# Kernel optimization log

Measured on AMD Instinct MI355X. Metric: run time of the kernel, lower is better.

The kernel has to match this reference:

```python
import jax, jax.numpy as jnp
import numpy as np

EPS = 1e-05
NEG = -1e9

def rotate_half(x):
    x1, x2 = jnp.split(x, 2, axis=-1)
    return jnp.concatenate([-x2, x1], axis=-1)

def rmsnorm(x, w):
    xf = x.astype(jnp.float32)
    n = xf * jax.lax.rsqrt(jnp.mean(xf * xf, axis=-1, keepdims=True) + EPS)
    return w * n.astype(x.dtype)

def setup_inputs() -> dict:
    key = jax.random.key(0)
    ks = jax.random.split(key, 12)
    B, S, H, NH, DH, FF = 1, 2048, 2048, 16, 128, 8192
    x = jax.random.normal(ks[0], (B, S, H), jnp.float32)
    # additive causal mask [1,1,S,S]
    causal = jnp.where(jnp.tril(jnp.ones((S, S), bool)), 0.0, NEG).astype(jnp.float32)
    attention_mask = causal[None, None]
    alibi = 0.1 * jax.random.normal(ks[1], (1, NH, S, S), jnp.float32)
    # rotary angles [S, DH]
    inv = 1.0 / (10000.0 ** (jnp.arange(0, DH, 2, dtype=jnp.float32) / DH))
    ang = jnp.arange(S, dtype=jnp.float32)[:, None] * inv[None, :]
    freqs = jnp.concatenate([ang, ang], axis=-1)  # [S, DH]
    sc = 1.0 / np.sqrt(H)
    wq = sc * jax.random.normal(ks[2], (H, H), jnp.float32)
    wk = sc * jax.random.normal(ks[3], (H, H), jnp.float32)
    wv = sc * jax.random.normal(ks[4], (H, H), jnp.float32)
    wo = sc * jax.random.normal(ks[5], (H, H), jnp.float32)
    w1 = sc * jax.random.normal(ks[6], (H, FF), jnp.float32)
    w3 = sc * jax.random.normal(ks[7], (H, FF), jnp.float32)
    w2 = (1.0 / np.sqrt(FF)) * jax.random.normal(ks[8], (FF, H), jnp.float32)
    attn_norm_w = jnp.ones((H,), jnp.float32)
    ffn_norm_w = jnp.ones((H,), jnp.float32)
    return dict(x=x, attention_mask=attention_mask, alibi=alibi, freqs=freqs,
                wq=wq, wk=wk, wv=wv, wo=wo, w1=w1, w2=w2, w3=w3,
                attn_norm_w=attn_norm_w, ffn_norm_w=ffn_norm_w)

def reference(x, attention_mask, alibi, freqs, wq, wk, wv, wo, w1, w2, w3,
              attn_norm_w, ffn_norm_w):
    B, S, H = x.shape
    NH = 16
    DH = H // NH
    nx = rmsnorm(x, attn_norm_w)
    # projections -> [B, NH, S, DH]
    def heads(y):
        return y.reshape(B, S, NH, DH).transpose(0, 2, 1, 3)
    q = heads(nx @ wq)
    k = heads(nx @ wk)
    v = heads(nx @ wv)
    cos, sin = jnp.cos(freqs), jnp.sin(freqs)  # [S, DH] broadcasts over B,NH
    q = q * cos + rotate_half(q) * sin
    k = k * cos + rotate_half(k) * sin
    scores = jnp.einsum('bhqd,bhkd->bhqk', q, k) / np.sqrt(DH)
    scores = scores + attention_mask + alibi
    attn = jax.nn.softmax(scores, axis=-1)
    out = jnp.einsum('bhqk,bhkd->bhqd', attn, v)
    out = out.transpose(0, 2, 1, 3).reshape(B, S, H)
    x = x + out @ wo
    nx = rmsnorm(x, ffn_norm_w)
    ff = (jax.nn.silu(nx @ w1) * (nx @ w3)) @ w2
    return x + ff
```

## Files before the change

### kernel.cpp

```cpp
#include <hip/hip_runtime.h>
#include <hip/hip_bf16.h>
#include <math.h>

typedef __bf16 bf16x8 __attribute__((ext_vector_type(8)));
typedef float  f32x4  __attribute__((ext_vector_type(4)));
typedef unsigned short u16x8 __attribute__((ext_vector_type(8)));

#define DEV static __device__ __forceinline__

DEV void gload16(const void* g, void* l) {
  __builtin_amdgcn_global_load_lds((__attribute__((address_space(1))) void*)g,
                                   (__attribute__((address_space(3))) void*)l,
                                   16, 0, 0);
}

DEV float bf2f(unsigned short u) {
  unsigned v = ((unsigned)u) << 16;
  return __builtin_bit_cast(float, v);
}
DEV unsigned short f2bf(float f) {
  unsigned u = __builtin_bit_cast(unsigned, f);
  u = u + 0x7fffu + ((u >> 16) & 1u);
  return (unsigned short)(u >> 16);
}

__global__ __launch_bounds__(256) void rmsnorm_k(const float* __restrict__ x,
    const float* __restrict__ w, unsigned short* __restrict__ out, int H) {
  int row = blockIdx.x;
  const float4* xr = (const float4*)(x + (size_t)row * H);
  float4 a = xr[threadIdx.x * 2], b = xr[threadIdx.x * 2 + 1];
  float ss = a.x*a.x + a.y*a.y + a.z*a.z + a.w*a.w
           + b.x*b.x + b.y*b.y + b.z*b.z + b.w*b.w;
#pragma unroll
  for (int o = 32; o; o >>= 1) ss += __shfl_down(ss, o, 64);
  __shared__ float red[4];
  if ((threadIdx.x & 63) == 0) red[threadIdx.x >> 6] = ss;
  __syncthreads();
  float rs = rsqrtf((red[0] + red[1] + red[2] + red[3]) * (1.0f / 2048.0f) + 1e-5f);
  size_t base = (size_t)row * H + threadIdx.x * 8;
  const float* wv = w + threadIdx.x * 8;
  float vals[8] = {a.x, a.y, a.z, a.w, b.x, b.y, b.z, b.w};
  u16x8 o8;
#pragma unroll
  for (int i = 0; i < 8; ++i) o8[i] = f2bf(vals[i] * rs * wv[i]);
  *(u16x8*)(out + base) = o8;
}

__global__ __launch_bounds__(256) void wtrans_k(const float* __restrict__ W,
    unsigned short* __restrict__ Wt, int R, int C) {
  __shared__ float tile[32][33];
  int c0 = blockIdx.x * 32, r0 = blockIdx.y * 32;
  int tx = threadIdx.x, ty = threadIdx.y;
#pragma unroll
  for (int i = 0; i < 4; ++i)
    tile[ty + i * 8][tx] = W[(size_t)(r0 + ty + i * 8) * C + c0 + tx];
  __syncthreads();
#pragma unroll
  for (int i = 0; i < 4; ++i)
    Wt[(size_t)(c0 + ty + i * 8) * R + r0 + tx] = f2bf(tile[tx][ty + i * 8]);
}


#define STG_A(H, BUF, KC) do {                                                 \
    gload16(Asrc0 + (size_t)(H) * 128 * lda + (KC),                            \
            &lds[(BUF) * 16384 + (H) * 8192 + w * 1024]);                      \
    gload16(Asrc1 + (size_t)(H) * 128 * lda + (KC),                            \
            &lds[(BUF) * 16384 + (H) * 8192 + w * 1024 + 512]);                \
  } while (0)

#define STG_B(H, BUF, KC) do {                                                 \
    gload16(Bsrc0 + (size_t)(H) * 128 * ldb + (KC),                            \
            &lds[32768 + (BUF) * 16384 + (H) * 8192 + w * 1024]);              \
    gload16(Bsrc1 + (size_t)(H) * 128 * ldb + (KC),                            \
            &lds[32768 + (BUF) * 16384 + (H) * 8192 + w * 1024 + 512]);        \
  } while (0)

#define DS_A(DST, MH) do {                                                     \
    const int abase = buf * 16384 + (MH) * 8192 + arow * 64;                   \
    _Pragma("unroll") for (int m = 0; m < 4; ++m) {                            \
      DST[m][0] = *(const bf16x8*)&lds[abase + m * 1024 + acol0];              \
      DST[m][1] = *(const bf16x8*)&lds[abase + m * 1024 + acol1];              \
    } } while (0)

#define DS_B(DST, NH) do {                                                     \
    const int bbase = 32768 + buf * 16384 + (NH) * 8192 + brow * 64;           \
    _Pragma("unroll") for (int n = 0; n < 2; ++n) {                            \
      DST[n][0] = *(const bf16x8*)&lds[bbase + n * 1024 + acol0];              \
      DST[n][1] = *(const bf16x8*)&lds[bbase + n * 1024 + acol1];              \
    } } while (0)

#define MFMA16(AI, AR, BR) do {                                                \
    __builtin_amdgcn_s_setprio(1);                                             \
    _Pragma("unroll") for (int m = 0; m < 4; ++m)                              \
      _Pragma("unroll") for (int n = 0; n < 2; ++n) {                          \
        acc[AI][m][n] = __builtin_amdgcn_mfma_f32_16x16x32_bf16(               \
            AR[m][0], BR[n][0], acc[AI][m][n], 0, 0, 0);                       \
        acc[AI][m][n] = __builtin_amdgcn_mfma_f32_16x16x32_bf16(               \
            AR[m][1], BR[n][1], acc[AI][m][n], 0, 0, 0);                       \
      }                                                                        \
    __builtin_amdgcn_s_setprio(0);                                             \
    __builtin_amdgcn_sched_barrier(0);                                         \
  } while (0)

#define SBAR_WAIT do {                                                         \
    __builtin_amdgcn_sched_barrier(0);                                         \
    __builtin_amdgcn_s_barrier();                                              \
    asm volatile("s_waitcnt lgkmcnt(0)" ::: "memory");                         \
  } while (0)

template <int EPI>
__global__ __launch_bounds__(512, 2) void gemm256_k(
    const unsigned short* __restrict__ A, int lda,
    const unsigned short* __restrict__ B, int ldb,
    unsigned short* __restrict__ Cb, float* __restrict__ Cf,
    int M, int N, int Kext) {
  __shared__ unsigned short lds[65536];
  const int t = threadIdx.x, w = t >> 6, lane = t & 63;
  const int nbm = M >> 8, nbn = N >> 8, nwg = nbm * nbn;
  int id = blockIdx.x;
  id = (id & 7) * (nwg >> 3) + (id >> 3);
  const int bm = id % nbm, bn = id / nbm;
  const size_t m0 = (size_t)bm << 8, n0 = (size_t)bn << 8;
  const int koff = blockIdx.y * Kext;
  const int NT = Kext >> 6;
  const int scol = ((lane & 7) ^ (lane >> 3)) * 8;
  const unsigned short* Asrc0 = A + (m0 + w * 16 + (lane >> 3)) * (size_t)lda + koff + scol;
  const unsigned short* Asrc1 = A + (m0 + w * 16 + 8 + (lane >> 3)) * (size_t)lda + koff + scol;
  const unsigned short* Bsrc0 = B + (n0 + w * 16 + (lane >> 3)) * (size_t)ldb + koff + scol;
  const unsigned short* Bsrc1 = B + (n0 + w * 16 + 8 + (lane >> 3)) * (size_t)ldb + koff + scol;
  const int arow = (w >> 2) * 64 + (lane & 15);
  const int brow = (w & 3) * 32 + (lane & 15);
  const int acol0 = ((lane >> 4) * 8) ^ ((lane & 7) << 3);
  const int acol1 = acol0 ^ 32;
  f32x4 acc[4][4][2] = {};
  bf16x8 Acur[4][2], B0r[2][2], B1r[2][2];
  STG_A(0, 0, 0); STG_B(0, 0, 0); STG_A(1, 0, 0); STG_B(1, 0, 0);
  STG_A(0, 1, 64); STG_B(0, 1, 64);
  asm volatile("s_waitcnt vmcnt(4)" ::: "memory");
  __builtin_amdgcn_s_barrier();
  for (int kt = 0; kt < NT; ++kt) {
    const int buf = kt & 1;
    const int kc1 = (kt + 1) * 64, kc2 = (kt + 2) * 64;
    const bool p1 = (kt + 1 < NT), p2 = (kt + 2 < NT);
    DS_A(Acur, 0); DS_B(B0r, 0);
    if (p1) STG_A(1, buf ^ 1, kc1);
    SBAR_WAIT;
    MFMA16(0, Acur, B0r);
    __builtin_amdgcn_s_barrier();
    DS_B(B1r, 1);
    if (p1) STG_B(1, buf ^ 1, kc1);
    SBAR_WAIT;
    MFMA16(1, Acur, B1r);
    __builtin_amdgcn_s_barrier();
    DS_A(Acur, 1);
    if (p2) STG_A(0, buf, kc2);
    SBAR_WAIT;
    MFMA16(3, Acur, B1r);
    __builtin_amdgcn_s_barrier();
    if (p2) STG_B(0, buf, kc2);
    __builtin_amdgcn_sched_barrier(0);
    __builtin_amdgcn_s_barrier();
    MFMA16(2, Acur, B0r);
    if (p2) { asm volatile("s_waitcnt vmcnt(4)" ::: "memory"); }
    else    { asm volatile("s_waitcnt vmcnt(0)" ::: "memory"); }
    __builtin_amdgcn_s_barrier();
  }
#pragma unroll
  for (int Mh = 0; Mh < 2; ++Mh)
#pragma unroll
    for (int Nh = 0; Nh < 2; ++Nh)
#pragma unroll
      for (int m = 0; m < 4; ++m)
#pragma unroll
        for (int n = 0; n < 2; ++n) {
          size_t gr = m0 + Mh * 128 + (w >> 2) * 64 + m * 16 + (lane >> 4) * 4;
          size_t gc = n0 + Nh * 128 + (w & 3) * 32 + n * 16 + (lane & 15);
          f32x4 v = acc[Mh * 2 + Nh][m][n];
#pragma unroll
          for (int j = 0; j < 4; ++j) {
            size_t o = (gr + j) * (size_t)N + gc;
            if constexpr (EPI == 0) Cb[o] = f2bf(v[j]);
            else Cf[(size_t)blockIdx.y * M * N + o] = v[j];
          }
        }
}

template <int EPI>
__global__ __launch_bounds__(256) void gemm_bt_k(
    const unsigned short* __restrict__ A, const unsigned short* __restrict__ B,
    float* __restrict__ Cf, unsigned short* __restrict__ Cb,
    const float* __restrict__ resid, int M, int N, int K) {
  constexpr int BK = 64;
  __shared__ unsigned short lA[128 * BK];
  __shared__ unsigned short lB[128 * BK];
  const int t = threadIdx.x, wave = t >> 6, lane = t & 63;
  int nwg = gridDim.x * gridDim.y;
  int id = blockIdx.y * gridDim.x + blockIdx.x;
  id = (id & 7) * (nwg >> 3) + (id >> 3);
  const int m0 = (id % gridDim.x) * 128, n0 = (id / gridDim.x) * 128;
  const int wr = (wave >> 1) * 64, wc = (wave & 1) * 64;
  f32x4 acc[4][4] = {};
  const int sr = t >> 3;
  const int sc = ((t & 7) ^ (sr & 7)) * 8;
  const unsigned short* Ab = A + (size_t)(m0 + sr) * K + sc;
  const unsigned short* Bb = B + (size_t)(n0 + sr) * K + sc;
  unsigned short* lAw = &lA[(wave * 8) * BK];
  unsigned short* lBw = &lB[(wave * 8) * BK];
  const int row = lane & 15, kg = (lane >> 4) * 8, swz = (lane & 7) << 3;
  for (int k0 = 0; k0 < K; k0 += BK) {
#pragma unroll
    for (int it = 0; it < 4; ++it) {
      gload16(Ab + (size_t)it * 32 * K + k0, lAw + it * 32 * BK);
      gload16(Bb + (size_t)it * 32 * K + k0, lBw + it * 32 * BK);
    }
    asm volatile("s_waitcnt vmcnt(0)" ::: "memory");
    __syncthreads();
#pragma unroll
    for (int kk = 0; kk < 2; ++kk) {
      bf16x8 af[4], bfr[4];
#pragma unroll
      for (int m = 0; m < 4; ++m)
        af[m] = *(const bf16x8*)&lA[(wr + m * 16 + row) * BK + ((kk * 32 + kg) ^ swz)];
#pragma unroll
      for (int n = 0; n < 4; ++n)
        bfr[n] = *(const bf16x8*)&lB[(wc + n * 16 + row) * BK + ((kk * 32 + kg) ^ swz)];
#pragma unroll
      for (int m = 0; m < 4; ++m)
#pragma unroll
        for (int n = 0; n < 4; ++n)
          acc[m][n] = __builtin_amdgcn_mfma_f32_16x16x32_bf16(af[m], bfr[n], acc[m][n], 0, 0, 0);
    }
    __syncthreads();
  }
  const int cg = lane >> 4, col = lane & 15;
#pragma unroll
  for (int m = 0; m < 4; ++m)
#pragma unroll
    for (int n = 0; n < 4; ++n) {
      int rr = m0 + wr + m * 16 + cg * 4;
      int cc = n0 + wc + n * 16 + col;
#pragma unroll
      for (int j = 0; j < 4; ++j) {
        float v = acc[m][n][j];
        size_t o = (size_t)(rr + j) * N + cc;
        if constexpr (EPI == 2) Cf[o] = v + resid[o];
        else if constexpr (EPI == 1) Cf[o] = v;
        else Cb[o] = f2bf(v);
      }
    }
}

__global__ __launch_bounds__(256) void rope_k(const unsigned short* __restrict__ qkv,
    const float* __restrict__ freqs, unsigned short* __restrict__ Qr,
    unsigned short* __restrict__ Kr, int S) {
  int idx = blockIdx.x * 256 + threadIdx.x;
  int dp = idx & 63, h = (idx >> 6) & 15, s = idx >> 10;
  float ang = freqs[s * 128 + dp];
  float c, sn;
  sincosf(ang, &sn, &c);
  size_t rq = (size_t)s * 6144 + h * 128 + dp;
  float q1 = bf2f(qkv[rq]),        q2 = bf2f(qkv[rq + 64]);
  float k1 = bf2f(qkv[rq + 2048]), k2 = bf2f(qkv[rq + 2048 + 64]);
  size_t ob = ((size_t)h * S + s) * 128 + dp;
  Qr[ob]      = f2bf(q1 * c - q2 * sn);
  Qr[ob + 64] = f2bf(q2 * c + q1 * sn);
  Kr[ob]      = f2bf(k1 * c - k2 * sn);
  Kr[ob + 64] = f2bf(k2 * c + k1 * sn);
}

__global__ __launch_bounds__(256) void vtrans_k(const unsigned short* __restrict__ qkv,
    unsigned short* __restrict__ Vt, int S) {
  __shared__ unsigned short tile[32][33];
  int h = blockIdx.z;
  int s0 = blockIdx.x * 32, d0 = blockIdx.y * 32;
  int tx = threadIdx.x, ty = threadIdx.y;
#pragma unroll
  for (int i = 0; i < 4; ++i)
    tile[ty + i * 8][tx] = qkv[(size_t)(s0 + ty + i * 8) * 6144 + 4096 + h * 128 + d0 + tx];
  __syncthreads();
#pragma unroll
  for (int i = 0; i < 4; ++i)
    Vt[((size_t)h * 128 + d0 + ty + i * 8) * S + s0 + tx] = tile[tx][ty + i * 8];
}

__global__ __launch_bounds__(256) void attn_k(
    const unsigned short* __restrict__ Qr, const unsigned short* __restrict__ Kr,
    const unsigned short* __restrict__ Vt, const float* __restrict__ alibi,
    unsigned short* __restrict__ Ao, int S) {
  const int DH = 128;
  __shared__ unsigned short lQ[64 * 128], lK[64 * 128], lV[128 * 64], lP[4 * 16 * 64];
  const int t = threadIdx.x, wave = t >> 6, lane = t & 63;
  const int h = blockIdx.y;
  const int nq = gridDim.x;
  const int bx = blockIdx.x;
  const int qt = (bx & 1) ? (nq - 1 - (bx >> 1)) : (bx >> 1);
  const int q0 = qt * 64;
  const int sr = t >> 4;
  const int scw = ((t & 15) ^ ((t >> 4) & 7)) * 8;
  const int vr = t >> 3;
  const int vcw = ((t & 7) ^ ((t >> 3) & 7)) * 8;
  const unsigned short* Qb = Qr + (size_t)h * S * DH;
  const unsigned short* Kb = Kr + (size_t)h * S * DH;
  const unsigned short* Vb = Vt + (size_t)h * DH * S;
#pragma unroll
  for (int it = 0; it < 4; ++it)
    gload16(Qb + (size_t)(q0 + it * 16 + sr) * DH + scw, &lQ[(it * 16 + wave * 4) * DH]);
  asm volatile("s_waitcnt vmcnt(0)" ::: "memory");
  __syncthreads();
  const int row = lane & 15, kg = (lane >> 4) * 8, cg = lane >> 4, col = lane & 15;
  const int kswz = (lane & 7) << 3;
  bf16x8 qf[4];
#pragma unroll
  for (int ks = 0; ks < 4; ++ks)
    qf[ks] = *(const bf16x8*)&lQ[(wave * 16 + row) * DH + ((ks * 32 + kg) ^ kswz)];
  f32x4 o[8] = {};
  float m_run[4] = {-1e30f, -1e30f, -1e30f, -1e30f};
  float l_run[4] = {};
  unsigned short* pw = &lP[wave * 16 * 64];
  const float scale = 0.08838834764831843f;
  const int ktiles = qt + 1;
  for (int kt = 0; kt < ktiles; ++kt) {
    int k0 = kt * 64;
#pragma unroll
    for (int it = 0; it < 4; ++it)
      gload16(Kb + (size_t)(k0 + it * 16 + sr) * DH + scw, &lK[(it * 16 + wave * 4) * DH]);
#pragma unroll
    for (int it = 0; it < 4; ++it)
      gload16(Vb + (size_t)(it * 32 + vr) * S + k0 + vcw, &lV[(it * 32 + wave * 8) * 64]);
    asm volatile("s_waitcnt vmcnt(4)" ::: "memory");
    __syncthreads();
    float al[4][4];
#pragma unroll
    for (int n = 0; n < 4; ++n) {
      int k_abs = k0 + n * 16 + col;
#pragma unroll
      for (int j = 0; j < 4; ++j) {
        int q_abs = q0 + wave * 16 + cg * 4 + j;
        al[n][j] = alibi[((size_t)h * S + q_abs) * S + k_abs];
      }
    }
    f32x4 sf[4] = {};
#pragma unroll
    for (int ks = 0; ks < 4; ++ks) {
      bf16x8 qv = qf[ks];
#pragma unroll
      for (int n = 0; n < 4; ++n) {
        bf16x8 kf = *(const bf16x8*)&lK[(n * 16 + row) * DH + ((ks * 32 + kg) ^ kswz)];
        sf[n] = __builtin_amdgcn_mfma_f32_16x16x32_bf16(qv, kf, sf[n], 0, 0, 0);
      }
    }
    float pv[4][4];
    float tmax[4] = {-1e30f, -1e30f, -1e30f, -1e30f};
#pragma unroll
    for (int n = 0; n < 4; ++n) {
      int k_abs = k0 + n * 16 + col;
#pragma unroll
      for (int j = 0; j < 4; ++j) {
        int q_abs = q0 + wave * 16 + cg * 4 + j;
        float v = sf[n][j] * scale + al[n][j];
        if (k_abs > q_abs) v = -1e30f;
        pv[n][j] = v;
        tmax[j] = fmaxf(tmax[j], v);
      }
    }
#pragma unroll
    for (int o2 = 1; o2 < 16; o2 <<= 1)
#pragma unroll
      for (int j = 0; j < 4; ++j) tmax[j] = fmaxf(tmax[j], __shfl_xor(tmax[j], o2, 64));
    float alpha[4], rsum[4] = {};
#pragma unroll
    for (int j = 0; j < 4; ++j) {
      float mn = fmaxf(m_run[j], tmax[j]);
      alpha[j] = __expf(m_run[j] - mn);
      m_run[j] = mn;
    }
#pragma unroll
    for (int n = 0; n < 4; ++n)
#pragma unroll
      for (int j = 0; j < 4; ++j) {
        float p = __expf(pv[n][j] - m_run[j]);
        pv[n][j] = p;
        rsum[j] += p;
      }
#pragma unroll
    for (int o2 = 1; o2 < 16; o2 <<= 1)
#pragma unroll
      for (int j = 0; j < 4; ++j) rsum[j] += __shfl_xor(rsum[j], o2, 64);
#pragma unroll
    for (int j = 0; j < 4; ++j) l_run[j] = l_run[j] * alpha[j] + rsum[j];
#pragma unroll
    for (int nn = 0; nn < 8; ++nn)
#pragma unroll
      for (int j = 0; j < 4; ++j) o[nn][j] *= alpha[j];
#pragma unroll
    for (int n = 0; n < 4; ++n)
#pragma unroll
      for (int j = 0; j < 4; ++j) {
        int pr = cg * 4 + j;
        pw[pr * 64 + ((n * 16 + col) ^ ((pr & 7) << 3))] = f2bf(pv[n][j]);
      }
    asm volatile("s_waitcnt vmcnt(0)" ::: "memory");
    __syncthreads();
#pragma unroll
    for (int kk = 0; kk < 2; ++kk) {
      bf16x8 pf = *(const bf16x8*)&pw[row * 64 + ((kk * 32 + kg) ^ kswz)];
#pragma unroll
      for (int nn = 0; nn < 8; ++nn) {
        bf16x8 vf = *(const bf16x8*)&lV[(nn * 16 + row) * 64 + ((kk * 32 + kg) ^ kswz)];
        o[nn] = __builtin_amdgcn_mfma_f32_16x16x32_bf16(pf, vf, o[nn], 0, 0, 0);
      }
    }
    __syncthreads();
  }
#pragma unroll
  for (int nn = 0; nn < 8; ++nn)
#pragma unroll
    for (int j = 0; j < 4; ++j) {
      int q_abs = q0 + wave * 16 + cg * 4 + j;
      Ao[(size_t)q_abs * 2048 + h * 128 + nn * 16 + col] = f2bf(o[nn][j] / l_run[j]);
    }
}

__global__ __launch_bounds__(256) void silumul2_k(const unsigned short* __restrict__ h13,
    unsigned short* __restrict__ g, long n8) {
  long i = (long)blockIdx.x * 256 + threadIdx.x;
  if (i >= n8) return;
  int rowi = (int)(i >> 10), c = (int)(i & 1023) * 8;
  u16x8 a = *(const u16x8*)(h13 + (size_t)rowi * 16384 + c);
  u16x8 b = *(const u16x8*)(h13 + (size_t)rowi * 16384 + 8192 + c);
  u16x8 r;
#pragma unroll
  for (int j = 0; j < 8; ++j) {
    float xx = bf2f(a[j]), yy = bf2f(b[j]);
    float s = xx / (1.0f + __expf(-xx));
    r[j] = f2bf(s * yy);
  }
  *(u16x8*)(g + i * 8) = r;
}

__global__ __launch_bounds__(256) void reduce4_k(const float* __restrict__ part,
    const float* __restrict__ resid, float* __restrict__ out, int n4, size_t mn) {
  int i = blockIdx.x * 256 + threadIdx.x;
  if (i >= n4) return;
  const float4* p = (const float4*)part;
  size_t q = mn >> 2;
  float4 a = ((const float4*)resid)[i];
  float4 s0 = p[i], s1 = p[i + q], s2 = p[i + 2 * q], s3 = p[i + 3 * q];
  float4 r;
  r.x = a.x + s0.x + s1.x + s2.x + s3.x;
  r.y = a.y + s0.y + s1.y + s2.y + s3.y;
  r.z = a.z + s0.z + s1.z + s2.z + s3.z;
  r.w = a.w + s0.w + s1.w + s2.w + s3.w;
  ((float4*)out)[i] = r;
}

extern "C" void kernel_launch(void* const* d_in, const int* in_sizes, int n_in,
                              void* d_out, int out_size, void* d_ws, size_t ws_size,
                              hipStream_t stream) {
  const int S = 2048, H = 2048, NH = 16, DH = 128, FF = 8192;
  const float* x     = (const float*)d_in[0];
  const float* alibi = (const float*)d_in[2];
  const float* freqs = (const float*)d_in[3];
  const float* wq    = (const float*)d_in[4];
  const float* wk    = (const float*)d_in[5];
  const float* wv    = (const float*)d_in[6];
  const float* wo    = (const float*)d_in[7];
  const float* w1    = (const float*)d_in[8];
  const float* w2    = (const float*)d_in[9];
  const float* w3    = (const float*)d_in[10];
  const float* anw   = (const float*)d_in[11];
  const float* fnw   = (const float*)d_in[12];
  float* out = (float*)d_out;

  char* ws = (char*)d_ws;
  size_t off = 0;
  auto alloc = [&](size_t n) { char* p = ws + off; off += (n + 255) & ~(size_t)255; return p; };
  unsigned short* qkvT = (unsigned short*)alloc((size_t)3 * H * H * 2);
  unsigned short* woT  = (unsigned short*)alloc((size_t)H * H * 2);
  unsigned short* w13T = (unsigned short*)alloc((size_t)2 * FF * H * 2);
  unsigned short* w2T  = (unsigned short*)alloc((size_t)H * FF * 2);
  float*          x2   = (float*)alloc((size_t)S * H * 4);
  unsigned short* nx2  = (unsigned short*)alloc((size_t)S * H * 2);
  unsigned short* gbuf = (unsigned short*)alloc((size_t)S * FF * 2);
  unsigned short* nx   = (unsigned short*)alloc((size_t)S * H * 2);
  unsigned short* qkvb = (unsigned short*)alloc((size_t)S * 3 * H * 2);
  unsigned short* Qr   = (unsigned short*)alloc((size_t)NH * S * DH * 2);
  unsigned short* Kr   = (unsigned short*)alloc((size_t)NH * S * DH * 2);
  unsigned short* Vt   = (unsigned short*)alloc((size_t)NH * DH * S * 2);
  unsigned short* attno= (unsigned short*)alloc((size_t)S * H * 2);
  unsigned short* h13  = nx;
  float* part = (float*)ws;

  dim3 tb32(32, 8);
  wtrans_k<<<dim3(64, 64), tb32, 0, stream>>>(wq, qkvT, H, H);
  wtrans_k<<<dim3(64, 64), tb32, 0, stream>>>(wk, qkvT + (size_t)H * H, H, H);
  wtrans_k<<<dim3(64, 64), tb32, 0, stream>>>(wv, qkvT + (size_t)2 * H * H, H, H);
  wtrans_k<<<dim3(64, 64), tb32, 0, stream>>>(wo, woT, H, H);
  wtrans_k<<<dim3(256, 64), tb32, 0, stream>>>(w1, w13T, H, FF);
  wtrans_k<<<dim3(256, 64), tb32, 0, stream>>>(w3, w13T + (size_t)FF * H, H, FF);
  wtrans_k<<<dim3(64, 256), tb32, 0, stream>>>(w2, w2T, FF, H);

  rmsnorm_k<<<S, 256, 0, stream>>>(x, anw, nx, H);
  gemm256_k<0><<<dim3(192, 1), 512, 0, stream>>>(nx, H, qkvT, H, qkvb, nullptr, S, 3 * H, H);
  rope_k<<<(S * NH * 64) / 256, 256, 0, stream>>>(qkvb, freqs, Qr, Kr, S);
  vtrans_k<<<dim3(S / 32, DH / 32, NH), tb32, 0, stream>>>(qkvb, Vt, S);
  attn_k<<<dim3(S / 64, NH), 256, 0, stream>>>(Qr, Kr, Vt, alibi, attno, S);
  gemm_bt_k<2><<<dim3(16, 16), 256, 0, stream>>>(attno, woT, x2, nullptr, x, S, H, H);
  rmsnorm_k<<<S, 256, 0, stream>>>(x2, fnw, nx2, H);
  gemm256_k<0><<<dim3(512, 1), 512, 0, stream>>>(nx2, H, w13T, H, h13, nullptr, S, 2 * FF, H);
  silumul2_k<<<8192, 256, 0, stream>>>(h13, gbuf, (long)S * FF / 8);
  gemm256_k<1><<<dim3(64, 4), 512, 0, stream>>>(gbuf, FF, w2T, FF, nullptr, part, S, H, H);
  reduce4_k<<<4096, 256, 0, stream>>>(part, x2, out, S * H / 4, (size_t)S * H);
}
```

Before: 568.7 us.

## Fuse SiLU-gate into W1/W3 GEMM epilogue and double-buffer attention K/V loads

Interleaves the transposed W1 and W3 rows in 16-row groups so each GEMM output tile holds matching gate and up columns. A new GEMM epilogue then applies SiLU and the multiply directly and writes the gated result, which removes the separate silumul kernel and the round trip of the 2×FF intermediate through memory. The attention kernel is also restructured to double-buffer K/V tiles in LDS and prefetch the next tile's alibi values into registers. Q is loaded straight from global memory into registers. This adds register pressure and more complex vmcnt accounting.

```diff
diff --git a/kernel.cpp b/kernel.cpp
--- a/kernel.cpp
+++ b/kernel.cpp
@@ -58,6 +58,23 @@
 #pragma unroll
   for (int i = 0; i < 4; ++i)
     Wt[(size_t)(c0 + ty + i * 8) * R + r0 + tx] = f2bf(tile[tx][ty + i * 8]);
+}
+
+__global__ __launch_bounds__(256) void wtrans_ilv_k(const float* __restrict__ W,
+    unsigned short* __restrict__ Wt, int R, int C, int half) {
+  __shared__ float tile[32][33];
+  int c0 = blockIdx.x * 32, r0 = blockIdx.y * 32;
+  int tx = threadIdx.x, ty = threadIdx.y;
+#pragma unroll
+  for (int i = 0; i < 4; ++i)
+    tile[ty + i * 8][tx] = W[(size_t)(r0 + ty + i * 8) * C + c0 + tx];
+  __syncthreads();
+#pragma unroll
+  for (int i = 0; i < 4; ++i) {
+    int c = c0 + ty + i * 8;
+    size_t dstrow = (size_t)(c >> 4) * 32 + (c & 15) + half * 16;
+    Wt[dstrow * R + r0 + tx] = f2bf(tile[tx][ty + i * 8]);
+  }
 }
 
 
@@ -170,19 +187,31 @@
 #pragma unroll
     for (int Nh = 0; Nh < 2; ++Nh)
 #pragma unroll
-      for (int m = 0; m < 4; ++m)
-#pragma unroll
-        for (int n = 0; n < 2; ++n) {
-          size_t gr = m0 + Mh * 128 + (w >> 2) * 64 + m * 16 + (lane >> 4) * 4;
-          size_t gc = n0 + Nh * 128 + (w & 3) * 32 + n * 16 + (lane & 15);
-          f32x4 v = acc[Mh * 2 + Nh][m][n];
+      for (int m = 0; m < 4; ++m) {
+        size_t gr = m0 + Mh * 128 + (w >> 2) * 64 + m * 16 + (lane >> 4) * 4;
+        if constexpr (EPI == 2) {
+          size_t gc = (n0 >> 1) + Nh * 64 + (w & 3) * 16 + (lane & 15);
+          f32x4 v0 = acc[Mh * 2 + Nh][m][0];
+          f32x4 v1 = acc[Mh * 2 + Nh][m][1];
 #pragma unroll
           for (int j = 0; j < 4; ++j) {
-            size_t o = (gr + j) * (size_t)N + gc;
-            if constexpr (EPI == 0) Cb[o] = f2bf(v[j]);
-            else Cf[(size_t)blockIdx.y * M * N + o] = v[j];
+            float s = v0[j] / (1.0f + __expf(-v0[j]));
+            Cb[(gr + j) * (size_t)(N >> 1) + gc] = f2bf(s * v1[j]);
+          }
+        } else {
+#pragma unroll
+          for (int n = 0; n < 2; ++n) {
+            size_t gc = n0 + Nh * 128 + (w & 3) * 32 + n * 16 + (lane & 15);
+            f32x4 v = acc[Mh * 2 + Nh][m][n];
+#pragma unroll
+            for (int j = 0; j < 4; ++j) {
+              size_t o = (gr + j) * (size_t)N + gc;
+              if constexpr (EPI == 0) Cb[o] = f2bf(v[j]);
+              else Cf[(size_t)blockIdx.y * M * N + o] = v[j];
+            }
           }
         }
+      }
 }
 
 template <int EPI>
@@ -283,134 +312,121 @@
     Vt[((size_t)h * 128 + d0 + ty + i * 8) * S + s0 + tx] = tile[tx][ty + i * 8];
 }
 
+
+#define STGKV(KT, BUF) do {                                                    \
+    _Pragma("unroll") for (int it = 0; it < 4; ++it)                           \
+      gload16(Kb + (size_t)((KT) * 64 + it * 16 + sr) * 128 + scw,             \
+              &lds[(BUF) * 8192 + (it * 16 + wave * 4) * 128]);                \
+    _Pragma("unroll") for (int it = 0; it < 4; ++it)                           \
+      gload16(Vb + (size_t)(it * 32 + vr) * S + (KT) * 64 + vcw,               \
+              &lds[16384 + (BUF) * 8192 + (it * 32 + wave * 8) * 64]);         \
+  } while (0)
+
+#define ATTN_TILE(CUR, NXT, KT) do {                                           \
+    const int buf = (KT) & 1;                                                  \
+    const bool p1 = ((KT) + 1 < ktiles);                                       \
+    if (p1) {                                                                  \
+      STGKV((KT) + 1, buf ^ 1);                                                \
+      _Pragma("unroll") for (int q8 = 0; q8 < 16; ++q8)                        \
+        NXT[q8] = albase[(size_t)(q8 & 3) * S + ((KT) + 1) * 64 + (q8 >> 2) * 16]; \
+      asm volatile("s_waitcnt vmcnt(24)" ::: "memory");                        \
+    } else {                                                                   \
+      asm volatile("s_waitcnt vmcnt(0)" ::: "memory");                         \
+    }                                                                          \
+    __builtin_amdgcn_s_barrier();                                              \
+    f32x4 sf[4] = {};                                                          \
+    _Pragma("unroll") for (int ks = 0; ks < 4; ++ks)                           \
+      _Pragma("unroll") for (int n = 0; n < 4; ++n) {                          \
+        bf16x8 kf = *(const bf16x8*)&lds[buf * 8192 + (n * 16 + row) * 128 +   \
+                                         ((ks * 32 + kg) ^ kswz)];             \
+        sf[n] = __builtin_amdgcn_mfma_f32_16x16x32_bf16(qf[ks], kf, sf[n], 0, 0, 0); \
+      }                                                                        \
+    float pv[4][4];                                                            \
+    float tmax[4] = {-1e30f, -1e30f, -1e30f, -1e30f};                          \
+    _Pragma("unroll") for (int n = 0; n < 4; ++n) {                            \
+      int k_abs = (KT) * 64 + n * 16 + col;                                    \
+      _Pragma("unroll") for (int j = 0; j < 4; ++j) {                          \
+        int q_abs = q0 + wave * 16 + cg * 4 + j;                               \
+        float v = sf[n][j] * scale + CUR[n * 4 + j];                           \
+        if (k_abs > q_abs) v = -1e30f;                                         \
+        pv[n][j] = v;                                                          \
+        tmax[j] = fmaxf(tmax[j], v);                                           \
+      } }                                                                      \
+    _Pragma("unroll") for (int o2 = 1; o2 < 16; o2 <<= 1)                      \
+      _Pragma("unroll") for (int j = 0; j < 4; ++j)                            \
+        tmax[j] = fmaxf(tmax[j], __shfl_xor(tmax[j], o2, 64));                 \
+    float alpha[4], rsum[4] = {};                                              \
+    _Pragma("unroll") for (int j = 0; j < 4; ++j) {                            \
+      float mn = fmaxf(m_run[j], tmax[j]);                                     \
+      alpha[j] = __expf(m_run[j] - mn);                                        \
+      m_run[j] = mn;                                                           \
+    }                                                                          \
+    _Pragma("unroll") for (int n = 0; n < 4; ++n)                              \
+      _Pragma("unroll") for (int j = 0; j < 4; ++j) {                          \
+        float p = __expf(pv[n][j] - m_run[j]);                                 \
+        pv[n][j] = p;                                                          \
+        rsum[j] += p;                                                          \
+      }                                                                        \
+    _Pragma("unroll") for (int o2 = 1; o2 < 16; o2 <<= 1)                      \
+      _Pragma("unroll") for (int j = 0; j < 4; ++j)                            \
+        rsum[j] += __shfl_xor(rsum[j], o2, 64);                                \
+    _Pragma("unroll") for (int j = 0; j < 4; ++j)                              \
+      l_run[j] = l_run[j] * alpha[j] + rsum[j];                                \
+    _Pragma("unroll") for (int nn = 0; nn < 8; ++nn)                           \
+      _Pragma("unroll") for (int j = 0; j < 4; ++j) o[nn][j] *= alpha[j];      \
+    _Pragma("unroll") for (int n = 0; n < 4; ++n)                              \
+      _Pragma("unroll") for (int j = 0; j < 4; ++j) {                          \
+        int pr = cg * 4 + j;                                                   \
+        pw[pr * 64 + ((n * 16 + col) ^ ((pr & 7) << 3))] = f2bf(pv[n][j]);     \
+      }                                                                        \
+    asm volatile("s_waitcnt lgkmcnt(0)" ::: "memory");                         \
+    __builtin_amdgcn_sched_barrier(0);                                         \
+    _Pragma("unroll") for (int kk = 0; kk < 2; ++kk) {                         \
+      bf16x8 pf = *(const bf16x8*)&pw[row * 64 + ((kk * 32 + kg) ^ kswz)];     \
+      _Pragma("unroll") for (int nn = 0; nn < 8; ++nn) {                       \
+        bf16x8 vf = *(const bf16x8*)&lds[16384 + buf * 8192 +                  \
+                                         (nn * 16 + row) * 64 +                \
+                                         ((kk * 32 + kg) ^ kswz)];             \
+        o[nn] = __builtin_amdgcn_mfma_f32_16x16x32_bf16(pf, vf, o[nn], 0, 0, 0); \
+      } }                                                                      \
+    __builtin_amdgcn_s_barrier();                                              \
+  } while (0)
+
 __global__ __launch_bounds__(256) void attn_k(
     const unsigned short* __restrict__ Qr, const unsigned short* __restrict__ Kr,
     const unsigned short* __restrict__ Vt, const float* __restrict__ alibi,
     unsigned short* __restrict__ Ao, int S) {
-  const int DH = 128;
-  __shared__ unsigned short lQ[64 * 128], lK[64 * 128], lV[128 * 64], lP[4 * 16 * 64];
+  __shared__ unsigned short lds[36864];
   const int t = threadIdx.x, wave = t >> 6, lane = t & 63;
-  const int h = blockIdx.y;
-  const int nq = gridDim.x;
-  const int bx = blockIdx.x;
+  const int h = blockIdx.y, nq = gridDim.x, bx = blockIdx.x;
   const int qt = (bx & 1) ? (nq - 1 - (bx >> 1)) : (bx >> 1);
   const int q0 = qt * 64;
-  const int sr = t >> 4;
-  const int scw = ((t & 15) ^ ((t >> 4) & 7)) * 8;
-  const int vr = t >> 3;
-  const int vcw = ((t & 7) ^ ((t >> 3) & 7)) * 8;
-  const unsigned short* Qb = Qr + (size_t)h * S * DH;
-  const unsigned short* Kb = Kr + (size_t)h * S * DH;
-  const unsigned short* Vb = Vt + (size_t)h * DH * S;
-#pragma unroll
-  for (int it = 0; it < 4; ++it)
-    gload16(Qb + (size_t)(q0 + it * 16 + sr) * DH + scw, &lQ[(it * 16 + wave * 4) * DH]);
-  asm volatile("s_waitcnt vmcnt(0)" ::: "memory");
-  __syncthreads();
+  const int sr = t >> 4, scw = ((t & 15) ^ ((t >> 4) & 7)) * 8;
+  const int vr = t >> 3, vcw = ((t & 7) ^ ((t >> 3) & 7)) * 8;
+  const unsigned short* Kb = Kr + (size_t)h * S * 128;
+  const unsigned short* Vb = Vt + (size_t)h * 128 * S;
   const int row = lane & 15, kg = (lane >> 4) * 8, cg = lane >> 4, col = lane & 15;
   const int kswz = (lane & 7) << 3;
   bf16x8 qf[4];
-#pragma unroll
-  for (int ks = 0; ks < 4; ++ks)
-    qf[ks] = *(const bf16x8*)&lQ[(wave * 16 + row) * DH + ((ks * 32 + kg) ^ kswz)];
+  const unsigned short* Qrow = Qr + ((size_t)h * S + q0 + wave * 16 + row) * 128;
+#pragma unroll
+  for (int ks = 0; ks < 4; ++ks) qf[ks] = *(const bf16x8*)&Qrow[ks * 32 + kg];
   f32x4 o[8] = {};
   float m_run[4] = {-1e30f, -1e30f, -1e30f, -1e30f};
   float l_run[4] = {};
-  unsigned short* pw = &lP[wave * 16 * 64];
+  unsigned short* pw = &lds[32768 + wave * 1024];
   const float scale = 0.08838834764831843f;
   const int ktiles = qt + 1;
-  for (int kt = 0; kt < ktiles; ++kt) {
-    int k0 = kt * 64;
-#pragma unroll
-    for (int it = 0; it < 4; ++it)
-      gload16(Kb + (size_t)(k0 + it * 16 + sr) * DH + scw, &lK[(it * 16 + wave * 4) * DH]);
-#pragma unroll
-    for (int it = 0; it < 4; ++it)
-      gload16(Vb + (size_t)(it * 32 + vr) * S + k0 + vcw, &lV[(it * 32 + wave * 8) * 64]);
-    asm volatile("s_waitcnt vmcnt(4)" ::: "memory");
-    __syncthreads();
-    float al[4][4];
-#pragma unroll
-    for (int n = 0; n < 4; ++n) {
-      int k_abs = k0 + n * 16 + col;
-#pragma unroll
-      for (int j = 0; j < 4; ++j) {
-        int q_abs = q0 + wave * 16 + cg * 4 + j;
-        al[n][j] = alibi[((size_t)h * S + q_abs) * S + k_abs];
-      }
-    }
-    f32x4 sf[4] = {};
-#pragma unroll
-    for (int ks = 0; ks < 4; ++ks) {
-      bf16x8 qv = qf[ks];
-#pragma unroll
-      for (int n = 0; n < 4; ++n) {
-        bf16x8 kf = *(const bf16x8*)&lK[(n * 16 + row) * DH + ((ks * 32 + kg) ^ kswz)];
-        sf[n] = __builtin_amdgcn_mfma_f32_16x16x32_bf16(qv, kf, sf[n], 0, 0, 0);
-      }
-    }
-    float pv[4][4];
-    float tmax[4] = {-1e30f, -1e30f, -1e30f, -1e30f};
-#pragma unroll
-    for (int n = 0; n < 4; ++n) {
-      int k_abs = k0 + n * 16 + col;
-#pragma unroll
-      for (int j = 0; j < 4; ++j) {
-        int q_abs = q0 + wave * 16 + cg * 4 + j;
-        float v = sf[n][j] * scale + al[n][j];
-        if (k_abs > q_abs) v = -1e30f;
-        pv[n][j] = v;
-        tmax[j] = fmaxf(tmax[j], v);
-      }
-    }
-#pragma unroll
-    for (int o2 = 1; o2 < 16; o2 <<= 1)
-#pragma unroll
-      for (int j = 0; j < 4; ++j) tmax[j] = fmaxf(tmax[j], __shfl_xor(tmax[j], o2, 64));
-    float alpha[4], rsum[4] = {};
-#pragma unroll
-    for (int j = 0; j < 4; ++j) {
-      float mn = fmaxf(m_run[j], tmax[j]);
-      alpha[j] = __expf(m_run[j] - mn);
-      m_run[j] = mn;
-    }
-#pragma unroll
-    for (int n = 0; n < 4; ++n)
-#pragma unroll
-      for (int j = 0; j < 4; ++j) {
-        float p = __expf(pv[n][j] - m_run[j]);
-        pv[n][j] = p;
-        rsum[j] += p;
-      }
-#pragma unroll
-    for (int o2 = 1; o2 < 16; o2 <<= 1)
-#pragma unroll
-      for (int j = 0; j < 4; ++j) rsum[j] += __shfl_xor(rsum[j], o2, 64);
-#pragma unroll
-    for (int j = 0; j < 4; ++j) l_run[j] = l_run[j] * alpha[j] + rsum[j];
-#pragma unroll
-    for (int nn = 0; nn < 8; ++nn)
-#pragma unroll
-      for (int j = 0; j < 4; ++j) o[nn][j] *= alpha[j];
-#pragma unroll
-    for (int n = 0; n < 4; ++n)
-#pragma unroll
-      for (int j = 0; j < 4; ++j) {
-        int pr = cg * 4 + j;
-        pw[pr * 64 + ((n * 16 + col) ^ ((pr & 7) << 3))] = f2bf(pv[n][j]);
-      }
-    asm volatile("s_waitcnt vmcnt(0)" ::: "memory");
-    __syncthreads();
-#pragma unroll
-    for (int kk = 0; kk < 2; ++kk) {
-      bf16x8 pf = *(const bf16x8*)&pw[row * 64 + ((kk * 32 + kg) ^ kswz)];
-#pragma unroll
-      for (int nn = 0; nn < 8; ++nn) {
-        bf16x8 vf = *(const bf16x8*)&lV[(nn * 16 + row) * 64 + ((kk * 32 + kg) ^ kswz)];
-        o[nn] = __builtin_amdgcn_mfma_f32_16x16x32_bf16(pf, vf, o[nn], 0, 0, 0);
-      }
-    }
-    __syncthreads();
+  const float* albase = alibi + (size_t)h * S * S +
+                        ((size_t)q0 + wave * 16 + cg * 4) * S + col;
+  float alA[16], alB[16];
+  STGKV(0, 0);
+#pragma unroll
+  for (int q8 = 0; q8 < 16; ++q8)
+    alA[q8] = albase[(size_t)(q8 & 3) * S + (q8 >> 2) * 16];
+  for (int kt = 0; kt < ktiles; kt += 2) {
+    ATTN_TILE(alA, alB, kt);
+    if (kt + 1 < ktiles) ATTN_TILE(alB, alA, kt + 1);
   }
 #pragma unroll
   for (int nn = 0; nn < 8; ++nn)
@@ -419,23 +435,6 @@
       int q_abs = q0 + wave * 16 + cg * 4 + j;
       Ao[(size_t)q_abs * 2048 + h * 128 + nn * 16 + col] = f2bf(o[nn][j] / l_run[j]);
     }
-}
-
-__global__ __launch_bounds__(256) void silumul2_k(const unsigned short* __restrict__ h13,
-    unsigned short* __restrict__ g, long n8) {
-  long i = (long)blockIdx.x * 256 + threadIdx.x;
-  if (i >= n8) return;
-  int rowi = (int)(i >> 10), c = (int)(i & 1023) * 8;
-  u16x8 a = *(const u16x8*)(h13 + (size_t)rowi * 16384 + c);
-  u16x8 b = *(const u16x8*)(h13 + (size_t)rowi * 16384 + 8192 + c);
-  u16x8 r;
-#pragma unroll
-  for (int j = 0; j < 8; ++j) {
-    float xx = bf2f(a[j]), yy = bf2f(b[j]);
-    float s = xx / (1.0f + __expf(-xx));
-    r[j] = f2bf(s * yy);
-  }
-  *(u16x8*)(g + i * 8) = r;
 }
 
 __global__ __launch_bounds__(256) void reduce4_k(const float* __restrict__ part,
@@ -488,7 +487,6 @@
   unsigned short* Kr   = (unsigned short*)alloc((size_t)NH * S * DH * 2);
   unsigned short* Vt   = (unsigned short*)alloc((size_t)NH * DH * S * 2);
   unsigned short* attno= (unsigned short*)alloc((size_t)S * H * 2);
-  unsigned short* h13  = nx;
   float* part = (float*)ws;
 
   dim3 tb32(32, 8);
@@ -496,8 +494,8 @@
   wtrans_k<<<dim3(64, 64), tb32, 0, stream>>>(wk, qkvT + (size_t)H * H, H, H);
   wtrans_k<<<dim3(64, 64), tb32, 0, stream>>>(wv, qkvT + (size_t)2 * H * H, H, H);
   wtrans_k<<<dim3(64, 64), tb32, 0, stream>>>(wo, woT, H, H);
-  wtrans_k<<<dim3(256, 64), tb32, 0, stream>>>(w1, w13T, H, FF);
-  wtrans_k<<<dim3(256, 64), tb32, 0, stream>>>(w3, w13T + (size_t)FF * H, H, FF);
+  wtrans_ilv_k<<<dim3(256, 64), tb32, 0, stream>>>(w1, w13T, H, FF, 0);
+  wtrans_ilv_k<<<dim3(256, 64), tb32, 0, stream>>>(w3, w13T, H, FF, 1);
   wtrans_k<<<dim3(64, 256), tb32, 0, stream>>>(w2, w2T, FF, H);
 
   rmsnorm_k<<<S, 256, 0, stream>>>(x, anw, nx, H);
@@ -507,8 +505,7 @@
   attn_k<<<dim3(S / 64, NH), 256, 0, stream>>>(Qr, Kr, Vt, alibi, attno, S);
   gemm_bt_k<2><<<dim3(16, 16), 256, 0, stream>>>(attno, woT, x2, nullptr, x, S, H, H);
   rmsnorm_k<<<S, 256, 0, stream>>>(x2, fnw, nx2, H);
-  gemm256_k<0><<<dim3(512, 1), 512, 0, stream>>>(nx2, H, w13T, H, h13, nullptr, S, 2 * FF, H);
-  silumul2_k<<<8192, 256, 0, stream>>>(h13, gbuf, (long)S * FF / 8);
+  gemm256_k<2><<<dim3(512, 1), 512, 0, stream>>>(nx2, H, w13T, H, gbuf, nullptr, S, 2 * FF, H);
   gemm256_k<1><<<dim3(64, 4), 512, 0, stream>>>(gbuf, FF, w2T, FF, nullptr, part, S, H, H);
   reduce4_k<<<4096, 256, 0, stream>>>(part, x2, out, S * H / 4, (size_t)S * H);
 }
```

Result: faster. 545.2 us (-4.1%).
